# Kernel optimization log

Hardware: AMD Instinct MI355X
Metric: run time of the kernel (lower is better)

The kernel has to match this reference:

```python
import jax, jax.numpy as jnp
import numpy as np

WINDOW_SIZE, SM, PS = 8, 2, 2  # window_size, spatial_merge_size, patch_size
SMU = SM * SM  # spatial_merge_unit


def _window_index(grid_thw):
    """Numpy port of get_window_index; returns permutation of arange(S)."""
    vmws = WINDOW_SIZE // SM // PS  # 2
    out, wid = [], 0
    for t, h, w in grid_thw:
        lh, lw = h // SM, w // SM
        idx = np.arange(t * lh * lw).reshape(t, lh, lw)
        ph = vmws - lh % vmws
        pw = vmws - lw % vmws
        nh, nw = (lh + ph) // vmws, (lw + pw) // vmws
        pad = np.full((t, lh + ph, lw + pw), -100, dtype=np.int64)
        pad[:, :lh, :lw] = idx
        pad = pad.reshape(t, nh, vmws, nw, vmws).transpose(0, 1, 3, 2, 4).reshape(-1)
        out.append(pad[pad != -100] + wid)
        wid += t * lh * lw
    return np.concatenate(out).astype(np.int32)


def setup_inputs() -> dict:
    key = jax.random.key(0)
    ks = jax.random.split(key, 5)
    B, T, C, H = 1, 16384, 1280, 16
    D = C // H  # 80
    grid_thw = np.array([[1, 256, 256]], dtype=np.int64)  # llm grid 128x128 -> S=16384
    wi = _window_index(grid_thw)
    x = jax.random.normal(ks[0], (B, T, C), jnp.float32)
    cos = jax.random.normal(ks[1], (B * T, 1, D), jnp.float32)
    sin = jax.random.normal(ks[2], (B * T, 1, D), jnp.float32)
    W_qkv = jax.random.normal(ks[3], (C, 3 * C), jnp.float32) * (C ** -0.5)
    W_proj = jax.random.normal(ks[4], (C, C), jnp.float32) * (C ** -0.5)
    # each window: (vmws*vmws) merged tokens * SMU patches = 16 tokens
    block_size = (WINDOW_SIZE // SM // PS) ** 2 * SMU
    return {"x": x, "cos": cos, "sin": sin, "W_qkv": W_qkv, "W_proj": W_proj,
            "window_index": jnp.asarray(wi), "block_size": block_size}


def reference(x, cos, sin, W_qkv, W_proj, window_index, block_size):
    B, T, C = x.shape
    S = B * T
    D = cos.shape[-1]
    H = C // D
    # window reorder (gather)
    xr = x.reshape(S, C)[window_index]
    qkv = (xr @ W_qkv).reshape(S, 3, H, D)
    q, k, v = qkv[:, 0], qkv[:, 1], qkv[:, 2]
    # module's (unusual) q/k mixing 'rotary'
    cw, sw = cos[window_index], sin[window_index]  # (S,1,D) broadcast over heads
    qr = q * cw + k * sw
    kr = k * cw - q * sw
    # block-diagonal attention: uniform 16-token windows -> reshape, no SxS mask
    nb = S // block_size
    qb = qr.reshape(nb, block_size, H, D)
    kb = kr.reshape(nb, block_size, H, D)
    vb = v.reshape(nb, block_size, H, D)
    att = jnp.einsum('bqhd,bkhd->bhqk', qb, kb) * (D ** -0.5)
    att = jax.nn.softmax(att, axis=-1)
    y = jnp.einsum('bhqk,bkhd->bqhd', att, vb).reshape(S, C)
    # undo window reorder
    y = y[jnp.argsort(window_index)]
    return y.reshape(B, T, C) @ W_proj
```

## Files before the change

kernel.cpp:

```cpp
#include <hip/hip_runtime.h>
#include <hip/hip_bf16.h>

#define S_TOK   16384
#define C_DIM   1280
#define C3_DIM  3840
#define H_DIM   16
#define D_DIM   80
#define BLK     16
#define PLANE_ELEMS ((size_t)S_TOK * C_DIM)

using u16x8  = __attribute__((ext_vector_type(8))) unsigned short;
using u16x4  = __attribute__((ext_vector_type(4))) unsigned short;
using bf16x8 = __attribute__((ext_vector_type(8))) __bf16;
using f32x4  = __attribute__((ext_vector_type(4))) float;

__device__ __forceinline__ unsigned short f2bf(float f) {
    return __bfloat16_as_ushort(__float2bfloat16(f));
}
__device__ __forceinline__ float bf2f(unsigned short u) {
    unsigned int x = (unsigned int)u << 16;
    return __builtin_bit_cast(float, x);
}
__device__ __forceinline__ void gload_lds16(const unsigned short* g, unsigned short* l) {
    __builtin_amdgcn_global_load_lds(
        (const __attribute__((address_space(1))) void*)g,
        (__attribute__((address_space(3))) void*)l, 16, 0, 0);
}

__global__ __launch_bounds__(256) void transpose_cvt(
    const float* __restrict__ W, unsigned short* __restrict__ WT, int K, int N)
{
    __shared__ float tile[32][33];
    const int n0 = blockIdx.x * 32, k0 = blockIdx.y * 32;
    const int tx = threadIdx.x & 31, ty = threadIdx.x >> 5;
#pragma unroll
    for (int i = ty; i < 32; i += 8)
        tile[i][tx] = W[(size_t)(k0 + i) * N + n0 + tx];
    __syncthreads();
#pragma unroll
    for (int i = ty; i < 32; i += 8)
        WT[(size_t)(n0 + i) * K + k0 + tx] = f2bf(tile[tx][i]);
}

__global__ __launch_bounds__(256) void gather_cvt(
    const float* __restrict__ x, const int* __restrict__ wi,
    unsigned short* __restrict__ xg)
{
    int idx = blockIdx.x * 256 + threadIdx.x;
    int s  = idx / 160;
    int c8 = (idx - s * 160) * 8;
    const float* src = x + (size_t)wi[s] * C_DIM + c8;
    f32x4 v0 = *(const f32x4*)src;
    f32x4 v1 = *(const f32x4*)(src + 4);
    u16x8 o;
    o[0]=f2bf(v0[0]); o[1]=f2bf(v0[1]); o[2]=f2bf(v0[2]); o[3]=f2bf(v0[3]);
    o[4]=f2bf(v1[0]); o[5]=f2bf(v1[1]); o[6]=f2bf(v1[2]); o[7]=f2bf(v1[3]);
    *(u16x8*)&xg[(size_t)s * C_DIM + c8] = o;
}

#define TM 128
#define TN 128
#define BK 64

template<int OUTMODE>
__global__ __launch_bounds__(256) void gemm_mfma(
    const unsigned short* __restrict__ A,
    const unsigned short* __restrict__ BT,
    void* __restrict__ Cp,
    int N, int K)
{
    __shared__ __align__(16) unsigned short As[TM * BK];
    __shared__ __align__(16) unsigned short Bs[TN * BK];

    const int m0   = blockIdx.x * TM;
    const int n0   = blockIdx.y * TN;
    const int tid  = threadIdx.x;
    const int lane = tid & 63;
    const int wv   = tid >> 6;
    const int wm   = (wv >> 1) * 64;
    const int wn   = (wv & 1) * 64;
    const int lrow = lane & 15;
    const int quad = lane >> 4;

    int r_[4], csw[4];
#pragma unroll
    for (int c = 0; c < 4; c++) {
        int ch = (wv * 4 + c) * 64 + lane;
        r_[c]  = ch >> 3;
        csw[c] = ((ch & 7) ^ (r_[c] & 7)) << 3;
    }

    int aoff[4], asw[4], boff[4], bsw[4];
#pragma unroll
    for (int t = 0; t < 4; t++) {
        int ra = wm + t * 16 + lrow;
        aoff[t] = ra << 7;  asw[t] = (ra & 7) << 4;
        int rb = wn + t * 16 + lrow;
        boff[t] = rb << 7;  bsw[t] = (rb & 7) << 4;
    }

    f32x4 acc[4][4];
#pragma unroll
    for (int i = 0; i < 4; i++)
#pragma unroll
        for (int j = 0; j < 4; j++)
            acc[i][j] = (f32x4){0.f, 0.f, 0.f, 0.f};

    for (int kt = 0; kt < K; kt += BK) {
#pragma unroll
        for (int c = 0; c < 4; c++)
            gload_lds16(A + (size_t)(m0 + r_[c]) * K + kt + csw[c],
                        As + (wv * 4 + c) * 512);
#pragma unroll
        for (int c = 0; c < 4; c++)
            gload_lds16(BT + (size_t)(n0 + r_[c]) * K + kt + csw[c],
                        Bs + (wv * 4 + c) * 512);
        __syncthreads();

#pragma unroll
        for (int ks = 0; ks < BK; ks += 32) {
            const int cb = (ks << 1) + (quad << 4);
            bf16x8 af[4], bfr[4];
#pragma unroll
            for (int mt = 0; mt < 4; mt++)
                af[mt] = *(const bf16x8*)((const char*)As +
                                          aoff[mt] + (cb ^ asw[mt]));
#pragma unroll
            for (int nt = 0; nt < 4; nt++)
                bfr[nt] = *(const bf16x8*)((const char*)Bs +
                                           boff[nt] + (cb ^ bsw[nt]));
#pragma unroll
            for (int mt = 0; mt < 4; mt++)
#pragma unroll
                for (int nt = 0; nt < 4; nt++)
                    acc[mt][nt] = __builtin_amdgcn_mfma_f32_16x16x32_bf16(
                        af[mt], bfr[nt], acc[mt][nt], 0, 0, 0);
        }
        __syncthreads();
    }

#pragma unroll
    for (int nt = 0; nt < 4; nt++) {
        const int cb = n0 + wn + nt * 16;
        unsigned short* pb = nullptr;
        if (OUTMODE == 2) {
            int which = cb / C_DIM;
            int hc    = cb - which * C_DIM;
            int h     = hc / D_DIM;
            int d0    = hc - h * D_DIM;
            pb = (unsigned short*)Cp + (size_t)which * PLANE_ELEMS
               + (size_t)h * S_TOK * D_DIM + d0 + lrow;
        }
#pragma unroll
        for (int mt = 0; mt < 4; mt++)
#pragma unroll
            for (int r = 0; r < 4; r++) {
                int row = m0 + wm + mt * 16 + quad * 4 + r;
                if (OUTMODE == 0)
                    ((float*)Cp)[(size_t)row * N + cb + lrow] = acc[mt][nt][r];
                else if (OUTMODE == 1)
                    ((unsigned short*)Cp)[(size_t)row * N + cb + lrow] =
                        f2bf(acc[mt][nt][r]);
                else
                    pb[(size_t)row * D_DIM] = f2bf(acc[mt][nt][r]);
            }
    }
}

__global__ __launch_bounds__(256) void attn_fused(
    const unsigned short* __restrict__ planes,
    const float* __restrict__ cosp,
    const float* __restrict__ sinp,
    const int* __restrict__ wi,
    unsigned short* __restrict__ y)
{
    const int wave = threadIdx.x >> 6;
    const int lane = threadIdx.x & 63;
    const int b    = blockIdx.y;
    const int h    = blockIdx.x * 4 + wave;
    const int j16  = lane & 15;
    const int quad = lane >> 4;

    const int srow = b * BLK + j16;
    const int crow = wi[srow];

    const unsigned short* Vb = planes + 2 * PLANE_ELEMS
        + ((size_t)h * S_TOK + b * BLK) * D_DIM + j16;
    u16x8 vraw[5];
#pragma unroll
    for (int t = 0; t < 5; t++) {
#pragma unroll
        for (int e = 0; e < 8; e++) {
            int kks = (quad < 2) ? (quad * 8 + e) : e;
            unsigned short rv = Vb[(size_t)kks * D_DIM + t * 16];
            vraw[t][e] = (quad < 2) ? rv : (unsigned short)0;
        }
    }

    const unsigned short* Qr = planes + ((size_t)h * S_TOK + srow) * D_DIM;
    const unsigned short* Kr = Qr + PLANE_ELEMS;
    const float* cr = cosp + (size_t)crow * D_DIM;
    const float* sr = sinp + (size_t)crow * D_DIM;
    bf16x8 qf[3], kf[3];
#pragma unroll
    for (int s = 0; s < 3; s++) {
        int d = 32 * s + quad * 8;
        bool valid = (d < D_DIM);
        int dc = valid ? d : 0;
        u16x8 qv = *(const u16x8*)(Qr + dc);
        u16x8 kv = *(const u16x8*)(Kr + dc);
        f32x4 c0 = *(const f32x4*)(cr + dc);
        f32x4 c1 = *(const f32x4*)(cr + dc + 4);
        f32x4 s0 = *(const f32x4*)(sr + dc);
        f32x4 s1 = *(const f32x4*)(sr + dc + 4);
        u16x8 qo, ko;
#pragma unroll
        for (int j = 0; j < 8; j++) {
            float cw = (j < 4) ? c0[j] : c1[j - 4];
            float sw = (j < 4) ? s0[j] : s1[j - 4];
            float q = bf2f(qv[j]), k = bf2f(kv[j]);
            qo[j] = valid ? f2bf(q * cw + k * sw) : (unsigned short)0;
            ko[j] = valid ? f2bf(k * cw - q * sw) : (unsigned short)0;
        }
        qf[s] = __builtin_bit_cast(bf16x8, qo);
        kf[s] = __builtin_bit_cast(bf16x8, ko);
    }

    f32x4 sacc = (f32x4){0.f, 0.f, 0.f, 0.f};
#pragma unroll
    for (int s = 0; s < 3; s++)
        sacc = __builtin_amdgcn_mfma_f32_16x16x32_bf16(kf[s], qf[s], sacc, 0, 0, 0);

    const float scale = 0.11180339887498948f;
    float sc[4];
#pragma unroll
    for (int r = 0; r < 4; r++) sc[r] = sacc[r] * scale;
    float m = fmaxf(fmaxf(sc[0], sc[1]), fmaxf(sc[2], sc[3]));
    m = fmaxf(m, __shfl_xor(m, 16));
    m = fmaxf(m, __shfl_xor(m, 32));
    float e[4], sum = 0.f;
#pragma unroll
    for (int r = 0; r < 4; r++) { e[r] = __expf(sc[r] - m); sum += e[r]; }
    sum += __shfl_xor(sum, 16);
    sum += __shfl_xor(sum, 32);
    float inv = 1.f / sum;

    int sl = quad * 32 + j16;
    float pv0[4], pv1[4];
#pragma unroll
    for (int r = 0; r < 4; r++) pv0[r] = __shfl(e[r], sl & 63);
#pragma unroll
    for (int r = 0; r < 4; r++) pv1[r] = __shfl(e[r], (sl + 16) & 63);
    u16x8 pf;
#pragma unroll
    for (int r = 0; r < 4; r++) {
        pf[r]     = (quad < 2) ? f2bf(pv0[r]) : (unsigned short)0;
        pf[r + 4] = (quad < 2) ? f2bf(pv1[r]) : (unsigned short)0;
    }
    bf16x8 pfrag = __builtin_bit_cast(bf16x8, pf);

    unsigned short* yrow = y + (size_t)crow * C_DIM + h * D_DIM + quad * 4;
#pragma unroll
    for (int t = 0; t < 5; t++) {
        f32x4 o = __builtin_amdgcn_mfma_f32_16x16x32_bf16(
            __builtin_bit_cast(bf16x8, vraw[t]), pfrag,
            (f32x4){0.f, 0.f, 0.f, 0.f}, 0, 0, 0);
        u16x4 ov;
#pragma unroll
        for (int r = 0; r < 4; r++) ov[r] = f2bf(o[r] * inv);
        *(u16x4*)(yrow + t * 16) = ov;
    }
}

extern "C" void kernel_launch(void* const* d_in, const int* in_sizes, int n_in,
                              void* d_out, int out_size, void* d_ws, size_t ws_size,
                              hipStream_t stream)
{
    const float* x     = (const float*)d_in[0];
    const float* cosp  = (const float*)d_in[1];
    const float* sinp  = (const float*)d_in[2];
    const float* Wqkv  = (const float*)d_in[3];
    const float* Wproj = (const float*)d_in[4];
    const int*   wi    = (const int*)d_in[5];

    char* ws = (char*)d_ws;
    unsigned short* planes = (unsigned short*)ws;
    unsigned short* yun    = (unsigned short*)(ws + 125829120ull);
    unsigned short* wqkvT  = (unsigned short*)(ws + 167772160ull);
    unsigned short* wprojT = (unsigned short*)(ws + 177602560ull);
    unsigned short* xg     = (unsigned short*)(ws + 180879360ull);

    transpose_cvt<<<dim3(C3_DIM / 32, C_DIM / 32), 256, 0, stream>>>(
        Wqkv, wqkvT, C_DIM, C3_DIM);
    transpose_cvt<<<dim3(C_DIM / 32, C_DIM / 32), 256, 0, stream>>>(
        Wproj, wprojT, C_DIM, C_DIM);

    gather_cvt<<<S_TOK * 160 / 256, 256, 0, stream>>>(x, wi, xg);

    gemm_mfma<2><<<dim3(S_TOK / TM, C3_DIM / TN), 256, 0, stream>>>(
        xg, wqkvT, planes, C3_DIM, C_DIM);

    attn_fused<<<dim3(H_DIM / 4, S_TOK / BLK), 256, 0, stream>>>(
        planes, cosp, sinp, wi, yun);

    gemm_mfma<0><<<dim3(S_TOK / TM, C_DIM / TN), 256, 0, stream>>>(
        yun, wprojT, d_out, C_DIM, C_DIM);
}
```

Baseline: 476.8 us.

## Stage attention operands through LDS and move the unpermute into the projection GEMM

The attention kernel now loads V into LDS through global_load_lds and builds the rotated Q/K in LDS with coalesced 16-byte chunk loads. Previously each lane issued scattered 2-byte V gathers and computed the rotation redundantly. Attention output is written in window order with contiguous rows instead of scattered by window index. The output projection GEMM scatters its rows through row_map (the window index) when storing. This trades a gathered bf16 write for a scattered fp32 row write in the final GEMM.

Result: no change. 477.4 us (+0.1%).

```diff
diff --git a/kernel.cpp b/kernel.cpp
--- a/kernel.cpp
+++ b/kernel.cpp
@@ -67,6 +67,7 @@
     const unsigned short* __restrict__ A,
     const unsigned short* __restrict__ BT,
     void* __restrict__ Cp,
+    const int* __restrict__ row_map,
     int N, int K)
 {
     __shared__ __align__(16) unsigned short As[TM * BK];
@@ -158,22 +159,26 @@
                 int row = m0 + wm + mt * 16 + quad * 4 + r;
                 if (OUTMODE == 0)
                     ((float*)Cp)[(size_t)row * N + cb + lrow] = acc[mt][nt][r];
-                else if (OUTMODE == 1)
-                    ((unsigned short*)Cp)[(size_t)row * N + cb + lrow] =
-                        f2bf(acc[mt][nt][r]);
+                else if (OUTMODE == 2)
+                    pb[(size_t)row * D_DIM] = f2bf(acc[mt][nt][r]);
                 else
-                    pb[(size_t)row * D_DIM] = f2bf(acc[mt][nt][r]);
+                    ((float*)Cp)[(size_t)row_map[row] * N + cb + lrow] =
+                        acc[mt][nt][r];
             }
     }
 }
 
-__global__ __launch_bounds__(256) void attn_fused(
+__global__ __launch_bounds__(256) void attn_v2(
     const unsigned short* __restrict__ planes,
     const float* __restrict__ cosp,
     const float* __restrict__ sinp,
     const int* __restrict__ wi,
-    unsigned short* __restrict__ y)
-{
+    unsigned short* __restrict__ yw)
+{
+    __shared__ __align__(16) unsigned short Q_lds[4][16][88];
+    __shared__ __align__(16) unsigned short K_lds[4][16][88];
+    __shared__ __align__(16) unsigned short V_lds[4][1536];
+
     const int wave = threadIdx.x >> 6;
     const int lane = threadIdx.x & 63;
     const int b    = blockIdx.y;
@@ -181,49 +186,57 @@
     const int j16  = lane & 15;
     const int quad = lane >> 4;
 
-    const int srow = b * BLK + j16;
-    const int crow = wi[srow];
-
-    const unsigned short* Vb = planes + 2 * PLANE_ELEMS
-        + ((size_t)h * S_TOK + b * BLK) * D_DIM + j16;
-    u16x8 vraw[5];
-#pragma unroll
-    for (int t = 0; t < 5; t++) {
-#pragma unroll
-        for (int e = 0; e < 8; e++) {
-            int kks = (quad < 2) ? (quad * 8 + e) : e;
-            unsigned short rv = Vb[(size_t)kks * D_DIM + t * 16];
-            vraw[t][e] = (quad < 2) ? rv : (unsigned short)0;
+    const unsigned short* Vsrc = planes + 2 * PLANE_ELEMS
+        + ((size_t)h * S_TOK + b * BLK) * D_DIM;
+    unsigned short* Vsl = &V_lds[wave][0];
+#pragma unroll
+    for (int c = 0; c < 3; c++)
+        gload_lds16(Vsrc + c * 512 + lane * 8, Vsl + c * 512);
+
+    const unsigned short* Qbase = planes + ((size_t)h * S_TOK + b * BLK) * D_DIM;
+#pragma unroll
+    for (int c = 0; c < 3; c++) {
+        int ch = c * 64 + lane;
+        if (ch < 160) {
+            int r  = ch / 10;
+            int d8 = (ch - r * 10) * 8;
+            int crow = wi[b * BLK + r];
+            const unsigned short* Qp = Qbase + (size_t)r * D_DIM + d8;
+            u16x8 qv = *(const u16x8*)Qp;
+            u16x8 kv = *(const u16x8*)(Qp + PLANE_ELEMS);
+            const float* cp = cosp + (size_t)crow * D_DIM + d8;
+            const float* sp = sinp + (size_t)crow * D_DIM + d8;
+            f32x4 c0 = *(const f32x4*)cp, c1 = *(const f32x4*)(cp + 4);
+            f32x4 s0 = *(const f32x4*)sp, s1 = *(const f32x4*)(sp + 4);
+            u16x8 qo, ko;
+#pragma unroll
+            for (int j = 0; j < 8; j++) {
+                float cw = (j < 4) ? c0[j] : c1[j - 4];
+                float sw = (j < 4) ? s0[j] : s1[j - 4];
+                float q = bf2f(qv[j]), k = bf2f(kv[j]);
+                qo[j] = f2bf(q * cw + k * sw);
+                ko[j] = f2bf(k * cw - q * sw);
+            }
+            *(u16x8*)&Q_lds[wave][r][d8] = qo;
+            *(u16x8*)&K_lds[wave][r][d8] = ko;
         }
     }
 
-    const unsigned short* Qr = planes + ((size_t)h * S_TOK + srow) * D_DIM;
-    const unsigned short* Kr = Qr + PLANE_ELEMS;
-    const float* cr = cosp + (size_t)crow * D_DIM;
-    const float* sr = sinp + (size_t)crow * D_DIM;
+    asm volatile("s_waitcnt vmcnt(0)" ::: "memory");
+    __builtin_amdgcn_sched_barrier(0);
+
+    const u16x8 zz = {0, 0, 0, 0, 0, 0, 0, 0};
     bf16x8 qf[3], kf[3];
 #pragma unroll
     for (int s = 0; s < 3; s++) {
-        int d = 32 * s + quad * 8;
-        bool valid = (d < D_DIM);
-        int dc = valid ? d : 0;
-        u16x8 qv = *(const u16x8*)(Qr + dc);
-        u16x8 kv = *(const u16x8*)(Kr + dc);
-        f32x4 c0 = *(const f32x4*)(cr + dc);
-        f32x4 c1 = *(const f32x4*)(cr + dc + 4);
-        f32x4 s0 = *(const f32x4*)(sr + dc);
-        f32x4 s1 = *(const f32x4*)(sr + dc + 4);
-        u16x8 qo, ko;
-#pragma unroll
-        for (int j = 0; j < 8; j++) {
-            float cw = (j < 4) ? c0[j] : c1[j - 4];
-            float sw = (j < 4) ? s0[j] : s1[j - 4];
-            float q = bf2f(qv[j]), k = bf2f(kv[j]);
-            qo[j] = valid ? f2bf(q * cw + k * sw) : (unsigned short)0;
-            ko[j] = valid ? f2bf(k * cw - q * sw) : (unsigned short)0;
-        }
-        qf[s] = __builtin_bit_cast(bf16x8, qo);
-        kf[s] = __builtin_bit_cast(bf16x8, ko);
+        int dcol = 32 * s + quad * 8;
+        bool pad = (dcol >= D_DIM);
+        int dc = pad ? 0 : dcol;
+        u16x8 qv = *(const u16x8*)&Q_lds[wave][j16][dc];
+        u16x8 kv = *(const u16x8*)&K_lds[wave][j16][dc];
+        if (pad) { qv = zz; kv = zz; }
+        qf[s] = __builtin_bit_cast(bf16x8, qv);
+        kf[s] = __builtin_bit_cast(bf16x8, kv);
     }
 
     f32x4 sacc = (f32x4){0.f, 0.f, 0.f, 0.f};
@@ -259,11 +272,23 @@
     }
     bf16x8 pfrag = __builtin_bit_cast(bf16x8, pf);
 
-    unsigned short* yrow = y + (size_t)crow * C_DIM + h * D_DIM + quad * 4;
+    u16x8 vf[5];
+#pragma unroll
+    for (int t = 0; t < 5; t++) {
+#pragma unroll
+        for (int e8 = 0; e8 < 8; e8++) {
+            int kks = quad * 8 + e8;
+            if (kks >= BLK) kks = e8;
+            vf[t][e8] = Vsl[kks * D_DIM + t * 16 + j16];
+        }
+    }
+
+    unsigned short* yrow = yw + (size_t)(b * BLK + j16) * C_DIM
+                         + h * D_DIM + quad * 4;
 #pragma unroll
     for (int t = 0; t < 5; t++) {
         f32x4 o = __builtin_amdgcn_mfma_f32_16x16x32_bf16(
-            __builtin_bit_cast(bf16x8, vraw[t]), pfrag,
+            __builtin_bit_cast(bf16x8, vf[t]), pfrag,
             (f32x4){0.f, 0.f, 0.f, 0.f}, 0, 0, 0);
         u16x4 ov;
 #pragma unroll
@@ -285,7 +310,7 @@
 
     char* ws = (char*)d_ws;
     unsigned short* planes = (unsigned short*)ws;
-    unsigned short* yun    = (unsigned short*)(ws + 125829120ull);
+    unsigned short* yw     = (unsigned short*)(ws + 125829120ull);
     unsigned short* wqkvT  = (unsigned short*)(ws + 167772160ull);
     unsigned short* wprojT = (unsigned short*)(ws + 177602560ull);
     unsigned short* xg     = (unsigned short*)(ws + 180879360ull);
@@ -298,11 +323,11 @@
     gather_cvt<<<S_TOK * 160 / 256, 256, 0, stream>>>(x, wi, xg);
 
     gemm_mfma<2><<<dim3(S_TOK / TM, C3_DIM / TN), 256, 0, stream>>>(
-        xg, wqkvT, planes, C3_DIM, C_DIM);
-
-    attn_fused<<<dim3(H_DIM / 4, S_TOK / BLK), 256, 0, stream>>>(
-        planes, cosp, sinp, wi, yun);
-
-    gemm_mfma<0><<<dim3(S_TOK / TM, C_DIM / TN), 256, 0, stream>>>(
-        yun, wprojT, d_out, C_DIM, C_DIM);
-}
+        xg, wqkvT, planes, nullptr, C3_DIM, C_DIM);
+
+    attn_v2<<<dim3(H_DIM / 4, S_TOK / BLK), 256, 0, stream>>>(
+        planes, cosp, sinp, wi, yw);
+
+    gemm_mfma<3><<<dim3(S_TOK / TM, C_DIM / TN), 256, 0, stream>>>(
+        yw, wprojT, d_out, wi, C_DIM, C_DIM);
+}
```
